# Kernel tuning notes

Hardware: AMD Instinct MI355X
Metric: run time of the kernel (lower is better)

The kernel has to match this reference:

```python
import jax, jax.numpy as jnp
import numpy as np

NF = 512
HEADS = 8
DHEAD = 64


def _dwconv(x, w):
    # x: [b, c, H, W], w: [c, 1, 3, 3] depthwise (groups=c), stride 1, pad 1
    return jax.lax.conv_general_dilated(
        x, w, window_strides=(1, 1), padding='SAME',
        feature_group_count=x.shape[1],
        dimension_numbers=('NCHW', 'OIHW', 'NCHW'))


def setup_inputs() -> dict:
    key = jax.random.key(0)
    ks = jax.random.split(key, 9)
    b, h, w, c = 4, 128, 128, NF
    hd = HEADS * DHEAD
    s = 1.0 / np.sqrt(c)
    return {
        'x_in': jax.random.normal(ks[0], (b, h, w, c), dtype=jnp.float32),
        'Wq': jax.random.normal(ks[1], (c, hd), dtype=jnp.float32) * s,
        'Wk': jax.random.normal(ks[2], (c, hd), dtype=jnp.float32) * s,
        'Wv': jax.random.normal(ks[3], (c, hd), dtype=jnp.float32) * s,
        'rescale': jnp.ones((HEADS, 1, 1), dtype=jnp.float32),
        'Wp': jax.random.normal(ks[4], (hd, c), dtype=jnp.float32) * s,
        'bp': jnp.zeros((c,), dtype=jnp.float32),
        'conv1_w': jax.random.normal(ks[5], (c, 1, 3, 3), dtype=jnp.float32) * (1.0 / 3.0),
        'conv2_w': jax.random.normal(ks[6], (c, 1, 3, 3), dtype=jnp.float32) * (1.0 / 3.0),
    }


def reference(x_in, Wq, Wk, Wv, rescale, Wp, bp, conv1_w, conv2_w):
    b, h, w, c = x_in.shape
    n = h * w
    x = x_in.reshape(b, n, c)
    # projections -> [b, heads, d, n] (transposed channel attention)
    def proj_t(W):
        return (x @ W).reshape(b, n, HEADS, DHEAD).transpose(0, 2, 3, 1)
    q = proj_t(Wq)
    k = proj_t(Wk)
    v_inp = x @ Wv  # [b, n, heads*d], kept for positional branch
    v = v_inp.reshape(b, n, HEADS, DHEAD).transpose(0, 2, 3, 1)
    # L2-normalize along token dim (last axis)
    qn = q / jnp.linalg.norm(q, axis=-1, keepdims=True)
    kn = k / jnp.linalg.norm(k, axis=-1, keepdims=True)
    # small d x d channel attention: attn = k @ q^T
    attn = jnp.einsum('bhdn,bhen->bhde', kn, qn) * rescale
    attn = jax.nn.softmax(attn, axis=-1)
    xo = jnp.einsum('bhde,bhen->bhdn', attn, v)
    xo = xo.transpose(0, 3, 1, 2).reshape(b, n, HEADS * DHEAD)
    out_c = (xo @ Wp + bp).reshape(b, h, w, c)
    # depthwise-conv positional branch on v_inp reshaped to image layout
    vimg = v_inp.reshape(b, h, w, c).transpose(0, 3, 1, 2)  # [b,c,h,w]
    y = _dwconv(vimg, conv1_w)
    y = jax.nn.gelu(y, approximate=False)  # F.gelu default is exact erf
    y = _dwconv(y, conv2_w)
    out_p = y.transpose(0, 2, 3, 1)
    return out_c + out_p
```

## Files before the change

### kernel.cpp

```cpp
#include <hip/hip_runtime.h>
#include <hip/hip_bf16.h>

typedef __attribute__((ext_vector_type(4))) float f32x4;
typedef __attribute__((ext_vector_type(8))) short s16x8;

__device__ __forceinline__ unsigned short f2bf(float f) {
    __hip_bfloat16 h = __float2bfloat16(f);
    return __builtin_bit_cast(unsigned short, h);
}
__device__ __forceinline__ float bf2f(unsigned short u) {
    return __builtin_bit_cast(float, ((unsigned)u) << 16);
}
__device__ __forceinline__ float2 bfpair(unsigned u) {
    float2 r;
    r.x = __builtin_bit_cast(float, u << 16);
    r.y = __builtin_bit_cast(float, u & 0xffff0000u);
    return r;
}
__device__ __forceinline__ void gload_lds16(const void* g, void* l) {
    __builtin_amdgcn_global_load_lds(
        (const __attribute__((address_space(1))) void*)g,
        (__attribute__((address_space(3))) void*)l, 16, 0, 0);
}
__device__ __forceinline__ float gelu_tanh(float x) {
    const float y = 0.7978845608028654f * (x + 0.044715f * x * x * x);
    const float t = __expf(-2.f * fabsf(y));
    const float th = (1.f - t) / (1.f + t);
    return 0.5f * x * (1.f + copysignf(th, y));
}

__global__ __launch_bounds__(256)
void k_cvt_tr(const float* __restrict__ in, unsigned short* __restrict__ XBF,
              unsigned short* __restrict__ XT) {
    __shared__ __align__(16) unsigned short tile[64 * 64];
    const int t  = threadIdx.x;
    const int c0 = blockIdx.x * 64;
    const int ty = blockIdx.y;
    const long tokg = (long)ty * 64;
    const int cq = t & 15, r0 = t >> 4;
#pragma unroll
    for (int p = 0; p < 4; ++p) {
        const int tok = r0 + p * 16;
        const float4 v = *(const float4*)(in + (tokg + tok) * 512 + c0 + cq * 4);
        union { unsigned short h[4]; uint2 u; } pk;
        pk.h[0] = f2bf(v.x); pk.h[1] = f2bf(v.y); pk.h[2] = f2bf(v.z); pk.h[3] = f2bf(v.w);
        *(uint2*)(XBF + (tokg + tok) * 512 + c0 + cq * 4) = pk.u;
        const int T = tok >> 3, i = tok & 7;
#pragma unroll
        for (int j = 0; j < 4; ++j) {
            const int c = cq * 4 + j;
            tile[c * 64 + ((T ^ (c & 7)) * 8 + i)] = pk.h[j];
        }
    }
    __syncthreads();
    const int b  = ty >> 8;
    const long tb = (long)(ty & 255) * 64;
    const int T2 = t & 7;
#pragma unroll
    for (int q = 0; q < 2; ++q) {
        const int c = (t >> 3) + q * 32;
        const uint4 v = *(const uint4*)&tile[c * 64 + ((T2 ^ (c & 7)) * 8)];
        *(uint4*)(XT + ((long)(b * 512 + c0 + c)) * 16384 + tb + T2 * 8) = v;
    }
}

__global__ __launch_bounds__(256)
void k_build_wcat(const float* __restrict__ Wq, const float* __restrict__ Wk,
                  const float* __restrict__ Wv, const float* __restrict__ Wp,
                  unsigned short* __restrict__ WcatT) {
    __shared__ float t[32][33];
    const int k0 = blockIdx.x * 32;
    const int j0 = blockIdx.y * 32;
    const float* src = (j0 < 512) ? Wq : (j0 < 1024 ? Wk : (j0 < 1536 ? Wv : Wp));
    const int jc0 = j0 & 511;
    const int r = threadIdx.x >> 5, c = threadIdx.x & 31;
#pragma unroll
    for (int rr = 0; rr < 4; ++rr) {
        const int k = k0 + r + rr * 8;
        t[c][r + rr * 8] = src[(long)k * 512 + jc0 + c];
    }
    __syncthreads();
#pragma unroll
    for (int rr = 0; rr < 4; ++rr) {
        const int j = j0 + r + rr * 8;
        WcatT[(long)j * 512 + k0 + c] = f2bf(t[r + rr * 8][c]);
    }
}

#define BM 128
#define BN 128
#define BK 64

template<int OUT_BF16, int BIAS, int ADDC>
__global__ __launch_bounds__(256, 2)
void gemm_mfma(const unsigned short* __restrict__ A, const unsigned short* __restrict__ B,
               void* __restrict__ C_, const float* __restrict__ bias,
               const unsigned short* __restrict__ addc,
               int lda, int ldb, int ldc, int K, long sA, long sB, long sC) {
    __shared__ __align__(16) unsigned short As[BM * BK];
    __shared__ __align__(16) unsigned short Bs[BN * BK];
    const int tid  = threadIdx.x;
    const int wave = tid >> 6;
    const int lane = tid & 63;
    const int wm = wave >> 1, wn = wave & 1;
    const int bm0 = blockIdx.y * BM;
    const int bn0 = blockIdx.x * BN;
    const long bz = blockIdx.z;
    A += bz * sA;
    B += bz * sB;

    const int l15 = lane & 15;
    const int l4  = lane >> 4;

    f32x4 acc[4][4];
#pragma unroll
    for (int i = 0; i < 4; ++i)
#pragma unroll
        for (int j = 0; j < 4; ++j) acc[i][j] = (f32x4){0.f, 0.f, 0.f, 0.f};

    const int srow    = wave * 8 + (lane >> 3);
    const int schunk0 = lane & 7;
    const int arow_b  = wm * 64 + l15;
    const int brow_b  = wn * 64 + l15;

    const int nk = K / BK;
    for (int kt = 0; kt < nk; ++kt) {
        const int k0 = kt * BK;
#pragma unroll
        for (int i = 0; i < 4; ++i) {
            const int r  = i * 32 + srow;
            const int gc = schunk0 ^ (r & 7);
            gload_lds16(A + (long)(bm0 + r) * lda + (k0 + gc * 8), &As[(i * 32 + wave * 8) * BK]);
            gload_lds16(B + (long)(bn0 + r) * ldb + (k0 + gc * 8), &Bs[(i * 32 + wave * 8) * BK]);
        }
        __syncthreads();
        s16x8 af[4][2], bfr[4][2];
#pragma unroll
        for (int mi = 0; mi < 4; ++mi) {
            const int row = arow_b + mi * 16;
#pragma unroll
            for (int ki = 0; ki < 2; ++ki) {
                const int ch = (ki * 4 + l4) ^ (row & 7);
                af[mi][ki] = *(const s16x8*)&As[row * BK + ch * 8];
            }
        }
#pragma unroll
        for (int ni = 0; ni < 4; ++ni) {
            const int row = brow_b + ni * 16;
#pragma unroll
            for (int ki = 0; ki < 2; ++ki) {
                const int ch = (ki * 4 + l4) ^ (row & 7);
                bfr[ni][ki] = *(const s16x8*)&Bs[row * BK + ch * 8];
            }
        }
#pragma unroll
        for (int ki = 0; ki < 2; ++ki)
#pragma unroll
            for (int mi = 0; mi < 4; ++mi)
#pragma unroll
                for (int ni = 0; ni < 4; ++ni)
                    acc[mi][ni] = __builtin_amdgcn_mfma_f32_16x16x32_bf16(
                        af[mi][ki], bfr[ni][ki], acc[mi][ni], 0, 0, 0);
        __syncthreads();
    }

#pragma unroll
    for (int mi = 0; mi < 4; ++mi) {
        const int row0 = bm0 + wm * 64 + mi * 16 + l4 * 4;
#pragma unroll
        for (int ni = 0; ni < 4; ++ni) {
            const int col = bn0 + wn * 64 + ni * 16 + l15;
            if (OUT_BF16) {
                unsigned short* C = (unsigned short*)C_ + bz * sC;
#pragma unroll
                for (int j = 0; j < 4; ++j)
                    C[(long)(row0 + j) * ldc + col] = f2bf(acc[mi][ni][j]);
            } else {
                float* C = (float*)C_ + bz * sC;
                const float bv = BIAS ? bias[col] : 0.f;
#pragma unroll
                for (int j = 0; j < 4; ++j) {
                    float v = acc[mi][ni][j] + bv;
                    if (ADDC) v += bf2f(addc[bz * sC + (long)(row0 + j) * ldc + col]);
                    C[(long)(row0 + j) * ldc + col] = v;
                }
            }
        }
    }
}

__global__ __launch_bounds__(256, 2)
void gemm_gram(const unsigned short* __restrict__ XT, float* __restrict__ P) {
    __shared__ __align__(16) unsigned short As[128 * 64];
    __shared__ __align__(16) unsigned short Bs[128 * 64];
    const int tid = threadIdx.x, wave = tid >> 6, lane = tid & 63;
    const int wm = wave >> 1, wn = wave & 1;
    const int bm0 = blockIdx.y * 128, bn0 = blockIdx.x * 128;
    const int z = blockIdx.z, b = z >> 3, chunk = z & 7;
    const unsigned short* A = XT + (long)b * 512 * 16384;
    const int l15 = lane & 15, l4 = lane >> 4;

    f32x4 acc[4][4];
#pragma unroll
    for (int i = 0; i < 4; ++i)
#pragma unroll
        for (int j = 0; j < 4; ++j) acc[i][j] = (f32x4){0.f, 0.f, 0.f, 0.f};

    const int srow = wave * 8 + (lane >> 3);
    const int sch  = lane & 7;
    const int arow_b = wm * 64 + l15;
    const int brow_b = wn * 64 + l15;

    for (int kt = 0; kt < 32; ++kt) {
        const long k0 = (long)chunk * 2048 + kt * 64;
#pragma unroll
        for (int i = 0; i < 4; ++i) {
            const int r  = i * 32 + srow;
            const int gc = sch ^ (r & 7);
            gload_lds16(A + (long)(bm0 + r) * 16384 + k0 + gc * 8, &As[(i * 32 + wave * 8) * 64]);
            gload_lds16(A + (long)(bn0 + r) * 16384 + k0 + gc * 8, &Bs[(i * 32 + wave * 8) * 64]);
        }
        __syncthreads();
        s16x8 af[4][2], bfr[4][2];
#pragma unroll
        for (int mi = 0; mi < 4; ++mi) {
            const int row = arow_b + mi * 16;
#pragma unroll
            for (int ki = 0; ki < 2; ++ki)
                af[mi][ki] = *(const s16x8*)&As[row * 64 + (((ki * 4 + l4) ^ (row & 7))) * 8];
        }
#pragma unroll
        for (int ni = 0; ni < 4; ++ni) {
            const int row = brow_b + ni * 16;
#pragma unroll
            for (int ki = 0; ki < 2; ++ki)
                bfr[ni][ki] = *(const s16x8*)&Bs[row * 64 + (((ki * 4 + l4) ^ (row & 7))) * 8];
        }
#pragma unroll
        for (int ki = 0; ki < 2; ++ki)
#pragma unroll
            for (int mi = 0; mi < 4; ++mi)
#pragma unroll
                for (int ni = 0; ni < 4; ++ni)
                    acc[mi][ni] = __builtin_amdgcn_mfma_f32_16x16x32_bf16(
                        af[mi][ki], bfr[ni][ki], acc[mi][ni], 0, 0, 0);
        __syncthreads();
    }

    float* Pb = P + ((long)((b * 8 + chunk) * 16 + blockIdx.y * 4 + blockIdx.x)) * 16384;
#pragma unroll
    for (int mi = 0; mi < 4; ++mi) {
        const int row0 = wm * 64 + mi * 16 + l4 * 4;
#pragma unroll
        for (int ni = 0; ni < 4; ++ni) {
            const int col = wn * 64 + ni * 16 + l15;
#pragma unroll
            for (int j = 0; j < 4; ++j)
                Pb[(row0 + j) * 128 + col] = acc[mi][ni][j];
        }
    }
}

__global__ void k_greduce(const float* __restrict__ P, unsigned* __restrict__ GB2) {
    const long idx = (long)blockIdx.x * 256 + threadIdx.x;
    const int b   = (int)(idx >> 17);
    const int rem = (int)(idx & 131071);
    const int c   = rem >> 8;
    const int cp0 = (rem & 255) * 2;
    const int tp  = (c >> 7) * 4 + (cp0 >> 7);
    const int e   = (c & 127) * 128 + (cp0 & 127);
    const float* Pp = P + ((long)(b * 8) * 16 + tp) * 16384 + e;
    float s0 = 0.f, s1 = 0.f;
#pragma unroll
    for (int ch = 0; ch < 8; ++ch) {
        const float2 v = *(const float2*)(Pp + (long)ch * 16 * 16384);
        s0 += v.x; s1 += v.y;
    }
    GB2[idx] = (unsigned)f2bf(s0) | ((unsigned)f2bf(s1) << 16);
}

__global__ void k_ssq(const unsigned short* __restrict__ WCT, const unsigned short* __restrict__ T1e,
                      const unsigned short* __restrict__ T2e, float* __restrict__ SSQ) {
    const int b = blockIdx.y;
    const int o = blockIdx.x * 256 + threadIdx.x;
    const unsigned short* wrow;
    const unsigned short* trow;
    if (o < 512) {
        wrow = WCT + (long)o * 512;
        trow = T1e + (long)b * 262144 + (long)o * 512;
    } else {
        const int d = o - 512;
        wrow = WCT + 262144 + (long)d * 512;
        trow = T2e + (long)b * 262144 + (long)d * 512;
    }
    float s = 0.f;
    for (int c = 0; c < 512; c += 8) {
        const s16x8 w = *(const s16x8*)&wrow[c];
        const s16x8 v = *(const s16x8*)&trow[c];
#pragma unroll
        for (int j = 0; j < 8; ++j)
            s += bf2f((unsigned short)w[j]) * bf2f((unsigned short)v[j]);
    }
    SSQ[b * 1024 + o] = s;
}

__global__ __launch_bounds__(256)
void k_softmax_bd(const float* __restrict__ attn, const float* __restrict__ sumsq,
                  const float* __restrict__ rescale, unsigned short* __restrict__ MBD) {
    __shared__ unsigned short TD[64 * 68];
    const int bh = blockIdx.x;
    const int b = bh >> 3, h = bh & 7;
    const int wave = threadIdx.x >> 6, e = threadIdx.x & 63;
    const float rs   = rescale[h];
    const float invq = rsqrtf(sumsq[b * 1024 + h * 64 + e]);
#pragma unroll 4
    for (int i = 0; i < 16; ++i) {
        const int d = wave * 16 + i;
        const float invk = rsqrtf(sumsq[b * 1024 + 512 + h * 64 + d]);
        const float v = attn[((long)b * 512 + h * 64 + d) * 512 + h * 64 + e] * invk * invq * rs;
        float mx = v;
#pragma unroll
        for (int off = 32; off >= 1; off >>= 1) mx = fmaxf(mx, __shfl_xor(mx, off));
        const float l = __expf(v - mx);
        float s = l;
#pragma unroll
        for (int off = 32; off >= 1; off >>= 1) s += __shfl_xor(s, off);
        TD[e * 68 + d] = f2bf(l / s);
    }
    __syncthreads();
    const int er = threadIdx.x >> 2, dc = (threadIdx.x & 3) * 16;
    union { unsigned short h[16]; uint4 u[2]; } pk;
#pragma unroll
    for (int j = 0; j < 16; ++j) pk.h[j] = TD[er * 68 + dc + j];
    uint4* dst = (uint4*)(MBD + ((long)b * 512 + h * 64 + er) * 512 + h * 64 + dc);
    dst[0] = pk.u[0];
    dst[1] = pk.u[1];
}

__global__ __launch_bounds__(256)
void k_conv1_gelu(const unsigned short* __restrict__ V,
                  const float* __restrict__ w, unsigned short* __restrict__ g) {
    const int x0 = blockIdx.x * 16;
    const int y  = blockIdx.y;
    const int b  = blockIdx.z;
    const int c0 = threadIdx.x * 2;
    float wq0[9], wq1[9];
#pragma unroll
    for (int i = 0; i < 9; ++i) { wq0[i] = w[c0 * 9 + i]; wq1[i] = w[(c0 + 1) * 9 + i]; }
    const long pixbase = (long)b * 16384;

    auto ld = [&](int yy, int xx) -> float2 {
        if (yy < 0 || yy > 127 || xx < 0 || xx > 127) return make_float2(0.f, 0.f);
        return bfpair(*(const unsigned*)(V + (pixbase + (long)yy * 128 + xx) * 512 + c0));
    };

    float2 col[3][6];
#pragma unroll
    for (int ky = 0; ky < 3; ++ky) {
        col[ky][0] = ld(y + ky - 1, x0 - 1);
        col[ky][1] = ld(y + ky - 1, x0);
    }
    for (int xq = 0; xq < 4; ++xq) {
        const int xb = x0 + xq * 4;
#pragma unroll
        for (int ky = 0; ky < 3; ++ky)
#pragma unroll
            for (int j = 0; j < 4; ++j)
                col[ky][2 + j] = ld(y + ky - 1, xb + 1 + j);
#pragma unroll
        for (int j = 0; j < 4; ++j) {
            float a0 = 0.f, a1 = 0.f;
#pragma unroll
            for (int ky = 0; ky < 3; ++ky)
#pragma unroll
                for (int kx = 0; kx < 3; ++kx) {
                    a0 += col[ky][j + kx].x * wq0[ky * 3 + kx];
                    a1 += col[ky][j + kx].y * wq1[ky * 3 + kx];
                }
            a0 = gelu_tanh(a0);
            a1 = gelu_tanh(a1);
            const unsigned up = (unsigned)f2bf(a0) | ((unsigned)f2bf(a1) << 16);
            *(unsigned*)(g + (pixbase + (long)y * 128 + xb + j) * 512 + c0) = up;
        }
#pragma unroll
        for (int ky = 0; ky < 3; ++ky) {
            col[ky][0] = col[ky][4];
            col[ky][1] = col[ky][5];
        }
    }
}

__global__ __launch_bounds__(256)
void k_conv2_bf(const unsigned short* __restrict__ gin,
                const float* __restrict__ w, unsigned short* __restrict__ outbf) {
    const int x0 = blockIdx.x * 16;
    const int y  = blockIdx.y;
    const int b  = blockIdx.z;
    const int c0 = threadIdx.x * 2;
    float wq0[9], wq1[9];
#pragma unroll
    for (int i = 0; i < 9; ++i) { wq0[i] = w[c0 * 9 + i]; wq1[i] = w[(c0 + 1) * 9 + i]; }
    const long pixbase = (long)b * 16384;

    auto ld = [&](int yy, int xx) -> float2 {
        if (yy < 0 || yy > 127 || xx < 0 || xx > 127) return make_float2(0.f, 0.f);
        return bfpair(*(const unsigned*)(gin + (pixbase + (long)yy * 128 + xx) * 512 + c0));
    };

    float2 col[3][6];
#pragma unroll
    for (int ky = 0; ky < 3; ++ky) {
        col[ky][0] = ld(y + ky - 1, x0 - 1);
        col[ky][1] = ld(y + ky - 1, x0);
    }
    for (int xq = 0; xq < 4; ++xq) {
        const int xb = x0 + xq * 4;
#pragma unroll
        for (int ky = 0; ky < 3; ++ky)
#pragma unroll
            for (int j = 0; j < 4; ++j)
                col[ky][2 + j] = ld(y + ky - 1, xb + 1 + j);
#pragma unroll
        for (int j = 0; j < 4; ++j) {
            float a0 = 0.f, a1 = 0.f;
#pragma unroll
            for (int ky = 0; ky < 3; ++ky)
#pragma unroll
                for (int kx = 0; kx < 3; ++kx) {
                    a0 += col[ky][j + kx].x * wq0[ky * 3 + kx];
                    a1 += col[ky][j + kx].y * wq1[ky * 3 + kx];
                }
            const unsigned up = (unsigned)f2bf(a0) | ((unsigned)f2bf(a1) << 16);
            *(unsigned*)(outbf + (pixbase + (long)y * 128 + xb + j) * 512 + c0) = up;
        }
#pragma unroll
        for (int ky = 0; ky < 3; ++ky) {
            col[ky][0] = col[ky][4];
            col[ky][1] = col[ky][5];
        }
    }
}

extern "C" void kernel_launch(void* const* d_in, const int* in_sizes, int n_in,
                              void* d_out, int out_size, void* d_ws, size_t ws_size,
                              hipStream_t stream) {
    const float* x_in    = (const float*)d_in[0];
    const float* Wq      = (const float*)d_in[1];
    const float* Wk      = (const float*)d_in[2];
    const float* Wv      = (const float*)d_in[3];
    const float* rescale = (const float*)d_in[4];
    const float* Wp      = (const float*)d_in[5];
    const float* bp      = (const float*)d_in[6];
    const float* c1w     = (const float*)d_in[7];
    const float* c2w     = (const float*)d_in[8];
    float* out = (float*)d_out;

    char* ws = (char*)d_ws;
    unsigned short* XBF = (unsigned short*)(ws);
    unsigned short* VBF = (unsigned short*)(ws + 67108864LL);
    unsigned short* XT  = (unsigned short*)(ws + 134217728LL);
    unsigned short* CV2 = XT;
    float*          P   = (float*)(ws + 201326592LL);
    unsigned short* WCT = (unsigned short*)(ws + 234881024LL);
    unsigned short* GB  = (unsigned short*)(ws + 236978176LL);
    unsigned short* T1e = (unsigned short*)(ws + 239075328LL);
    unsigned short* T2e = (unsigned short*)(ws + 241172480LL);
    float*          SSQ = (float*)(ws + 243269632LL);
    float*          ATTF= (float*)(ws + 243286016LL);
    unsigned short* MBD = (unsigned short*)(ws + 247480320LL);
    unsigned short* WEF = (unsigned short*)(ws + 249577472LL);

    (void)hipMemsetAsync(MBD, 0, 2097152, stream);

    k_cvt_tr<<<dim3(8, 1024), dim3(256), 0, stream>>>(x_in, XBF, XT);
    k_build_wcat<<<dim3(16, 64), dim3(256), 0, stream>>>(Wq, Wk, Wv, Wp, WCT);

    gemm_mfma<1, 0, 0><<<dim3(4, 512, 1), dim3(256), 0, stream>>>(
        XBF, WCT + 2 * 262144, (void*)VBF, nullptr, nullptr, 512, 512, 512, 512, 0L, 0L, 0L);

    gemm_gram<<<dim3(4, 4, 32), dim3(256), 0, stream>>>(XT, P);
    k_greduce<<<dim3(2048), dim3(256), 0, stream>>>(P, (unsigned*)GB);

    gemm_mfma<1, 0, 0><<<dim3(4, 4, 4), dim3(256), 0, stream>>>(
        WCT + 262144, GB, (void*)T2e, nullptr, nullptr, 512, 512, 512, 512, 0L, 262144L, 262144L);
    gemm_mfma<1, 0, 0><<<dim3(4, 4, 4), dim3(256), 0, stream>>>(
        WCT, GB, (void*)T1e, nullptr, nullptr, 512, 512, 512, 512, 0L, 262144L, 262144L);
    gemm_mfma<0, 0, 0><<<dim3(4, 4, 4), dim3(256), 0, stream>>>(
        T2e, WCT, (void*)ATTF, nullptr, nullptr, 512, 512, 512, 512, 262144L, 0L, 262144L);

    k_ssq<<<dim3(4, 4), dim3(256), 0, stream>>>(WCT, T1e, T2e, SSQ);
    k_softmax_bd<<<dim3(32), dim3(256), 0, stream>>>(ATTF, SSQ, rescale, MBD);

    gemm_mfma<1, 0, 0><<<dim3(4, 4, 4), dim3(256), 0, stream>>>(
        WCT + 3 * 262144, MBD, (void*)WEF, nullptr, nullptr, 512, 512, 512, 512, 0L, 262144L, 262144L);

    k_conv1_gelu<<<dim3(8, 128, 4), dim3(256), 0, stream>>>(VBF, c1w, XBF);
    k_conv2_bf<<<dim3(8, 128, 4), dim3(256), 0, stream>>>(XBF, c2w, CV2);

    gemm_mfma<0, 1, 1><<<dim3(4, 128, 4), dim3(256), 0, stream>>>(
        VBF, WEF, (void*)out, bp, CV2, 512, 512, 512, 512,
        (long)16384 * 512, 262144L, (long)16384 * 512);
}
```

Baseline: 395.5 us.

## Exploit Gram symmetry, remap GEMM block order, and stage epilogue stores through LDS

The Gram GEMM now computes only the upper-triangular 128x128 tiles (10 of 16) and writes each off-diagonal tile twice, once transposed. This removes almost half of its MFMA work and its X^T reads. The generic GEMM permutes the linear block index across groups of 8, likely to spread neighbouring tiles over XCDs or cache. Its epilogue also goes through shared memory to emit coalesced 16-byte stores instead of scattered scalar stores. The costs are extra LDS round trips and barriers in the epilogue, and strided transposed writes in the Gram kernel.

```diff
diff --git a/kernel.cpp b/kernel.cpp
--- a/kernel.cpp
+++ b/kernel.cpp
@@ -97,15 +97,25 @@
                void* __restrict__ C_, const float* __restrict__ bias,
                const unsigned short* __restrict__ addc,
                int lda, int ldb, int ldc, int K, long sA, long sB, long sC) {
-    __shared__ __align__(16) unsigned short As[BM * BK];
-    __shared__ __align__(16) unsigned short Bs[BN * BK];
+    __shared__ __align__(16) unsigned short sm[BM * BK * 2];
+    unsigned short* As = sm;
+    unsigned short* Bs = sm + BM * BK;
+
     const int tid  = threadIdx.x;
     const int wave = tid >> 6;
     const int lane = tid & 63;
     const int wm = wave >> 1, wn = wave & 1;
-    const int bm0 = blockIdx.y * BM;
-    const int bn0 = blockIdx.x * BN;
-    const long bz = blockIdx.z;
+
+    const int nx = gridDim.x, ny = gridDim.y;
+    const int nwg = nx * ny * gridDim.z;
+    int lid = blockIdx.x + nx * (blockIdx.y + ny * blockIdx.z);
+    lid = (lid & 7) * (nwg >> 3) + (lid >> 3);
+    const int bxi = lid % nx;
+    const int rest = lid / nx;
+    const int byi = rest % ny;
+    const long bz = rest / ny;
+    const int bm0 = byi * BM;
+    const int bn0 = bxi * BN;
     A += bz * sA;
     B += bz * sB;
 
@@ -164,26 +174,67 @@
         __syncthreads();
     }
 
-#pragma unroll
-    for (int mi = 0; mi < 4; ++mi) {
-        const int row0 = bm0 + wm * 64 + mi * 16 + l4 * 4;
-#pragma unroll
-        for (int ni = 0; ni < 4; ++ni) {
-            const int col = bn0 + wn * 64 + ni * 16 + l15;
-            if (OUT_BF16) {
-                unsigned short* C = (unsigned short*)C_ + bz * sC;
-#pragma unroll
-                for (int j = 0; j < 4; ++j)
-                    C[(long)(row0 + j) * ldc + col] = f2bf(acc[mi][ni][j]);
-            } else {
-                float* C = (float*)C_ + bz * sC;
-                const float bv = BIAS ? bias[col] : 0.f;
-#pragma unroll
-                for (int j = 0; j < 4; ++j) {
-                    float v = acc[mi][ni][j] + bv;
-                    if (ADDC) v += bf2f(addc[bz * sC + (long)(row0 + j) * ldc + col]);
-                    C[(long)(row0 + j) * ldc + col] = v;
+    if (OUT_BF16) {
+        unsigned short* Cs = sm;
+        unsigned short* C = (unsigned short*)C_ + bz * sC;
+#pragma unroll
+        for (int pass = 0; pass < 2; ++pass) {
+            __syncthreads();
+            if (wn == pass) {
+#pragma unroll
+                for (int mi = 0; mi < 4; ++mi)
+#pragma unroll
+                    for (int ni = 0; ni < 4; ++ni)
+#pragma unroll
+                        for (int j = 0; j < 4; ++j)
+                            Cs[(wm * 64 + mi * 16 + l4 * 4 + j) * 64 + ni * 16 + l15] =
+                                f2bf(acc[mi][ni][j]);
+            }
+            __syncthreads();
+            const int colL = (tid & 7) * 8;
+#pragma unroll
+            for (int it = 0; it < 4; ++it) {
+                const int row = it * 32 + (tid >> 3);
+                const uint4 v = *(const uint4*)&Cs[row * 64 + colL];
+                *(uint4*)&C[(long)(bm0 + row) * ldc + bn0 + pass * 64 + colL] = v;
+            }
+        }
+    } else {
+        float* Cs = (float*)sm;
+        float* C = (float*)C_ + bz * sC;
+#pragma unroll
+        for (int pass = 0; pass < 2; ++pass) {
+            __syncthreads();
+            if (wn == pass) {
+#pragma unroll
+                for (int mi = 0; mi < 4; ++mi)
+#pragma unroll
+                    for (int ni = 0; ni < 4; ++ni)
+#pragma unroll
+                        for (int j = 0; j < 4; ++j)
+                            Cs[(wm * 64 + mi * 16 + l4 * 4 + j) * 64 + ni * 16 + l15] =
+                                acc[mi][ni][j];
+            }
+            __syncthreads();
+            const int colL = (tid & 15) * 4;
+#pragma unroll
+            for (int it = 0; it < 8; ++it) {
+                const int row = it * 16 + (tid >> 4);
+                f32x4 v = *(const f32x4*)&Cs[row * 64 + colL];
+                const long gr = bm0 + row;
+                const int gc = bn0 + pass * 64 + colL;
+                if (BIAS) {
+                    const float4 bv = *(const float4*)(bias + gc);
+                    v[0] += bv.x; v[1] += bv.y; v[2] += bv.z; v[3] += bv.w;
                 }
+                if (ADDC) {
+                    const uint2 a2 = *(const uint2*)(addc + bz * sC + gr * ldc + gc);
+                    v[0] += bf2f((unsigned short)(a2.x & 0xffff));
+                    v[1] += bf2f((unsigned short)(a2.x >> 16));
+                    v[2] += bf2f((unsigned short)(a2.y & 0xffff));
+                    v[3] += bf2f((unsigned short)(a2.y >> 16));
+                }
+                *(f32x4*)&C[gr * ldc + gc] = v;
             }
         }
     }
@@ -195,8 +246,14 @@
     __shared__ __align__(16) unsigned short Bs[128 * 64];
     const int tid = threadIdx.x, wave = tid >> 6, lane = tid & 63;
     const int wm = wave >> 1, wn = wave & 1;
-    const int bm0 = blockIdx.y * 128, bn0 = blockIdx.x * 128;
-    const int z = blockIdx.z, b = z >> 3, chunk = z & 7;
+    const int p = blockIdx.x;
+    int ti, tj;
+    if (p < 4)      { ti = 0; tj = p; }
+    else if (p < 7) { ti = 1; tj = p - 3; }
+    else if (p < 9) { ti = 2; tj = p - 5; }
+    else            { ti = 3; tj = 3; }
+    const int bm0 = ti * 128, bn0 = tj * 128;
+    const int z = blockIdx.y, b = z >> 3, chunk = z & 7;
     const unsigned short* A = XT + (long)b * 512 * 16384;
     const int l15 = lane & 15, l4 = lane >> 4;
 
@@ -247,7 +304,8 @@
         __syncthreads();
     }
 
-    float* Pb = P + ((long)((b * 8 + chunk) * 16 + blockIdx.y * 4 + blockIdx.x)) * 16384;
+    const long zbase = (long)(b * 8 + chunk) * 16;
+    float* Pb = P + (zbase + ti * 4 + tj) * 16384;
 #pragma unroll
     for (int mi = 0; mi < 4; ++mi) {
         const int row0 = wm * 64 + mi * 16 + l4 * 4;
@@ -257,6 +315,18 @@
 #pragma unroll
             for (int j = 0; j < 4; ++j)
                 Pb[(row0 + j) * 128 + col] = acc[mi][ni][j];
+        }
+    }
+    if (ti != tj) {
+        float* Pt = P + (zbase + tj * 4 + ti) * 16384;
+#pragma unroll
+        for (int mi = 0; mi < 4; ++mi) {
+            const int row0 = wm * 64 + mi * 16 + l4 * 4;
+#pragma unroll
+            for (int ni = 0; ni < 4; ++ni) {
+                const int col = wn * 64 + ni * 16 + l15;
+                *(f32x4*)&Pt[(long)col * 128 + row0] = acc[mi][ni];
+            }
         }
     }
 }
@@ -478,7 +548,7 @@
     gemm_mfma<1, 0, 0><<<dim3(4, 512, 1), dim3(256), 0, stream>>>(
         XBF, WCT + 2 * 262144, (void*)VBF, nullptr, nullptr, 512, 512, 512, 512, 0L, 0L, 0L);
 
-    gemm_gram<<<dim3(4, 4, 32), dim3(256), 0, stream>>>(XT, P);
+    gemm_gram<<<dim3(10, 32), dim3(256), 0, stream>>>(XT, P);
     k_greduce<<<dim3(2048), dim3(256), 0, stream>>>(P, (unsigned*)GB);
 
     gemm_mfma<1, 0, 0><<<dim3(4, 4, 4), dim3(256), 0, stream>>>(
```

Measured after the change: 396.1 us. About the same (+0.1%).
